# Kernel optimization log

Hardware: AMD Instinct MI355X
Metric: run time of the kernel (lower is better)

Reference implementation:

```python
import jax, jax.numpy as jnp
import numpy as np

S = 4096            # num tokens (single causal sequence)
HID = 1024          # hidden_size
NH = 16             # num query heads
NKV = 4             # num kv heads
HD = 64             # head_dim
THETA = 10000.0
Q_SIZE = NH * HD
KV_SIZE = NKV * HD


def setup_inputs() -> dict:
    key = jax.random.key(0)
    k1, k2, k3 = jax.random.split(key, 3)
    return {
        "positions": jnp.arange(S, dtype=jnp.int32),
        "hidden_states": jax.random.normal(k1, (S, 2 * HID), dtype=jnp.float32),
        "w_qkv": jax.random.normal(k2, (Q_SIZE + 2 * KV_SIZE, 2 * HID), dtype=jnp.float32) * 0.02,
        "w_o": jax.random.normal(k3, (HID, Q_SIZE), dtype=jnp.float32) * 0.02,
    }


def _rope(x, positions):
    # x: [S, H, HD]; neox-style rotate-half RoPE
    half = HD // 2
    inv_freq = 1.0 / (THETA ** (jnp.arange(0, half, dtype=jnp.float32) / half))
    freqs = positions.astype(jnp.float32)[:, None] * inv_freq  # [S, half]
    cos = jnp.cos(freqs)[:, None, :]  # [S, 1, half]
    sin = jnp.sin(freqs)[:, None, :]
    x1, x2 = x[..., :half], x[..., half:]
    return jnp.concatenate([x1 * cos - x2 * sin, x2 * cos + x1 * sin], axis=-1)


def reference(positions, hidden_states, w_qkv, w_o):
    qkv = hidden_states @ w_qkv.T  # [S, Q_SIZE + 2*KV_SIZE]
    q = qkv[:, :Q_SIZE].reshape(S, NH, HD)
    k = qkv[:, Q_SIZE:Q_SIZE + KV_SIZE].reshape(S, NKV, HD)
    v = qkv[:, Q_SIZE + KV_SIZE:].reshape(S, NKV, HD)
    q = _rope(q, positions)
    k = _rope(k, positions)
    # GQA: group query heads over kv heads
    g = NH // NKV
    qg = q.reshape(S, NKV, g, HD)
    scale = HD ** -0.5
    scores = jnp.einsum("qhgd,thd->hgqt", qg, k) * scale  # [NKV, g, S, S]
    causal = positions[:, None] >= positions[None, :]      # [S, S]
    scores = jnp.where(causal[None, None], scores, jnp.finfo(scores.dtype).min)
    probs = jax.nn.softmax(scores, axis=-1)
    o = jnp.einsum("hgqt,thd->qhgd", probs, v).reshape(S, Q_SIZE)
    return o @ w_o.T  # [S, HID]
```

## Files before the change

### kernel.cpp

```cpp
#include <hip/hip_runtime.h>
#include <math.h>

#define S_LEN   4096
#define NHEADS  16
#define NKVH    4
#define HDIM    64
#define QKV_N   1536
#define HID2    2048
#define OUT_N   1024

typedef __attribute__((ext_vector_type(8))) __bf16 bf16x8;
typedef __attribute__((ext_vector_type(4))) __bf16 bf16x4;
typedef __attribute__((ext_vector_type(4))) float  f32x4;
typedef __attribute__((ext_vector_type(16))) float f32x16;
typedef __attribute__((ext_vector_type(4))) unsigned int u32x4;

#define GL_LDS16(gaddr, laddr)                                                  \
  __builtin_amdgcn_global_load_lds(                                             \
      (const __attribute__((address_space(1))) unsigned int*)(gaddr),           \
      (__attribute__((address_space(3))) unsigned int*)(laddr), 16, 0, 0)

__device__ __forceinline__ unsigned cvt_pk_bf16(float lo, float hi) {
  unsigned r;
  asm("v_cvt_pk_bf16_f32 %0, %1, %2" : "=v"(r) : "v"(lo), "v"(hi));
  return r;
}

__global__ __launch_bounds__(256) void cvt_all(const float* __restrict__ hid,
                                               const float* __restrict__ wq,
                                               const float* __restrict__ wo,
                                               __bf16* __restrict__ hid_bf,
                                               __bf16* __restrict__ wq_bf,
                                               __bf16* __restrict__ wo_bf) {
  const int n1 = S_LEN * HID2;
  const int n2 = QKV_N * HID2;
  int i = (blockIdx.x * blockDim.x + threadIdx.x) * 8;
  const float* src; __bf16* dst; int off;
  if (i < n1)           { src = hid; dst = hid_bf; off = i; }
  else if (i < n1 + n2) { src = wq;  dst = wq_bf;  off = i - n1; }
  else                  { src = wo;  dst = wo_bf;  off = i - n1 - n2; }
  float4 a = *(const float4*)(src + off);
  float4 b = *(const float4*)(src + off + 4);
  bf16x8 o = {(__bf16)a.x,(__bf16)a.y,(__bf16)a.z,(__bf16)a.w,
              (__bf16)b.x,(__bf16)b.y,(__bf16)b.z,(__bf16)b.w};
  *(bf16x8*)(dst + off) = o;
}

__global__ __launch_bounds__(256) void rope_table(const int* __restrict__ positions,
                                                  float* __restrict__ ct,
                                                  float* __restrict__ st) {
  int i = blockIdx.x * blockDim.x + threadIdx.x;
  int s = i >> 5, d = i & 31;
  double inv = pow(10000.0, -(double)d / 32.0);
  double fr = (double)positions[s] * inv;
  ct[i] = (float)cos(fr);
  st[i] = (float)sin(fr);
}

template<int BM, bool C_BF16>
__global__ __launch_bounds__(256) void gemm_m97(const __bf16* __restrict__ A,
                                                const __bf16* __restrict__ B,
                                                void* __restrict__ Cp,
                                                int M, int N, int K) {
  constexpr int TM = BM / 32;
  __shared__ __align__(16) __bf16 As[BM * 32];
  __shared__ __align__(16) __bf16 Bs[128 * 32];
  const int tid  = threadIdx.x;
  const int bm   = blockIdx.x, bn = blockIdx.y;
  const int wave = tid >> 6, lane = tid & 63;
  const int quad = lane >> 4, col = lane & 15;
  const int wm = (wave >> 1) * (BM / 2), wn = (wave & 1) * 64;

  const int lrow = lane >> 2, lcol = (lane & 3) * 8;
  const __bf16* Ag = A + (size_t)(bm * BM + wave * (BM / 4) + lrow) * K + lcol;
  const __bf16* Bg = B + (size_t)(bn * 128 + wave * 32 + lrow) * K + lcol;
  __bf16* AsW = As + wave * (BM / 4) * 32;
  __bf16* BsW = Bs + wave * 32 * 32;

  f32x4 acc[TM][4];
#pragma unroll
  for (int i = 0; i < TM; ++i)
#pragma unroll
    for (int j = 0; j < 4; ++j) acc[i][j] = (f32x4){0.f, 0.f, 0.f, 0.f};

  for (int kk = 0; kk < K; kk += 32) {
    __syncthreads();
#pragma unroll
    for (int u = 0; u < BM / 64; ++u)
      GL_LDS16(Ag + kk + (size_t)(u * 16) * K, AsW + u * 16 * 32);
    GL_LDS16(Bg + kk,                  BsW);
    GL_LDS16(Bg + kk + (size_t)16 * K, BsW + 16 * 32);
    __syncthreads();

    bf16x8 a[TM], b[4];
#pragma unroll
    for (int tm = 0; tm < TM; ++tm)
      a[tm] = *(const bf16x8*)&As[(wm + tm * 16 + col) * 32 + quad * 8];
#pragma unroll
    for (int tn = 0; tn < 4; ++tn)
      b[tn] = *(const bf16x8*)&Bs[(wn + tn * 16 + col) * 32 + quad * 8];
#pragma unroll
    for (int tm = 0; tm < TM; ++tm)
#pragma unroll
      for (int tn = 0; tn < 4; ++tn)
        acc[tm][tn] = __builtin_amdgcn_mfma_f32_16x16x32_bf16(a[tm], b[tn], acc[tm][tn], 0, 0, 0);
  }

#pragma unroll
  for (int tm = 0; tm < TM; ++tm)
#pragma unroll
    for (int tn = 0; tn < 4; ++tn) {
      int row = bm * BM + wm + tm * 16 + quad * 4;
      int cg  = bn * 128 + wn + tn * 16 + col;
#pragma unroll
      for (int r = 0; r < 4; ++r) {
        if constexpr (C_BF16)
          ((__bf16*)Cp)[(size_t)(row + r) * N + cg] = (__bf16)acc[tm][tn][r];
        else
          ((float*)Cp)[(size_t)(row + r) * N + cg] = acc[tm][tn][r];
      }
    }
}

__global__ __launch_bounds__(256) void rope_cast(const __bf16* __restrict__ qkv,
                                                 const float* __restrict__ ct,
                                                 const float* __restrict__ st,
                                                 __bf16* __restrict__ qb,
                                                 __bf16* __restrict__ kb) {
  int g = blockIdx.x * blockDim.x + threadIdx.x;
  int d = g & 31;
  int rem = g >> 5;
  int head = rem % 20;
  int s = rem / 20;
  bool isq = head < NHEADS;
  const __bf16* src = qkv + (size_t)s * QKV_N + (isq ? head * 64 : 1024 + (head - 16) * 64);
  float c  = ct[s * 32 + d];
  float sn = st[s * 32 + d];
  float x1 = (float)src[d], x2 = (float)src[d + 32];
  float y1 = x1 * c - x2 * sn;
  float y2 = x2 * c + x1 * sn;
  float scl = isq ? 0.125f : 1.0f;
  __bf16* dst = isq ? (qb + (size_t)s * 1024 + head * 64)
                    : (kb + (size_t)s * 256 + (head - 16) * 64);
  dst[d]      = (__bf16)(y1 * scl);
  dst[d + 32] = (__bf16)(y2 * scl);
}

__global__ __launch_bounds__(256) void v_transpose(const __bf16* __restrict__ qkv,
                                                   __bf16* __restrict__ vT) {
  __shared__ __align__(16) __bf16 Ts[64][72];
  const int sb = blockIdx.x, kvh = blockIdx.y, t = threadIdx.x;
  const int r = t >> 2, c16 = (t & 3) * 16;
  const __bf16* src = qkv + (size_t)(sb * 64 + r) * QKV_N + 1280 + kvh * 64 + c16;
  bf16x8 v0 = *(const bf16x8*)src;
  bf16x8 v1 = *(const bf16x8*)(src + 8);
#pragma unroll
  for (int u = 0; u < 8; ++u) {
    Ts[c16 + u][r]     = v0[u];
    Ts[c16 + 8 + u][r] = v1[u];
  }
  __syncthreads();
  __bf16* dst = vT + ((size_t)kvh * 64 + r) * S_LEN + sb * 64 + c16;
  *(bf16x8*)dst       = *(const bf16x8*)&Ts[r][c16];
  *(bf16x8*)(dst + 8) = *(const bf16x8*)&Ts[r][c16 + 8];
}

__global__ __launch_bounds__(256, 4) void attn_split(const __bf16* __restrict__ qg,
                                                     const __bf16* __restrict__ kg,
                                                     const __bf16* __restrict__ vg,
                                                     __bf16* __restrict__ op0,
                                                     __bf16* __restrict__ op1,
                                                     float* __restrict__ lp) {
  __shared__ __align__(16) __bf16 lds[18432];
  __bf16* Ks = lds;
  __bf16* Vs = lds + 9216;

  const int tid = threadIdx.x;
  const int h = blockIdx.x;
  const int yy = blockIdx.y;
  const int qq = yy >> 1, split = yy & 1;
  const int qb = (qq < 16) ? qq : 47 - qq;
  const int kvh = h >> 2;
  const int wave = tid >> 6, lane = tid & 63;
  const int r31 = lane & 31, hi = lane >> 5;
  const int hi4 = hi * 4, hi8 = hi * 8;
  const int qbase = qb * 128 + wave * 32;
  const int kt0 = split * (qb + 1);
  const int ktEnd = kt0 + qb + 1;

  {
    const int r = tid >> 1, c = (tid & 1) * 32;
    const __bf16* src = qg + (size_t)(qb * 128 + r) * 1024 + h * 64 + c;
    __bf16* dq = lds + r * 72 + c;
    *(bf16x8*)(dq)      = *(const bf16x8*)(src);
    *(bf16x8*)(dq + 8)  = *(const bf16x8*)(src + 8);
    *(bf16x8*)(dq + 16) = *(const bf16x8*)(src + 16);
    *(bf16x8*)(dq + 24) = *(const bf16x8*)(src + 24);
  }

  const int sr = tid >> 2, sc = (tid & 3) * 16;
  const __bf16* kptr = kg + (size_t)sr * 256 + kvh * 64 + sc;
  const __bf16* vptr = vg + ((size_t)kvh * 64 + sr) * S_LEN + sc;
  bf16x8 kr0 = *(const bf16x8*)(kptr + (size_t)kt0 * 64 * 256);
  bf16x8 kr1 = *(const bf16x8*)(kptr + (size_t)kt0 * 64 * 256 + 8);
  bf16x8 vr0 = *(const bf16x8*)(vptr + (size_t)kt0 * 64);
  bf16x8 vr1 = *(const bf16x8*)(vptr + (size_t)kt0 * 64 + 8);

  __syncthreads();

  bf16x8 qf[4];
#pragma unroll
  for (int dc = 0; dc < 4; ++dc)
    qf[dc] = *(const bf16x8*)&lds[(wave * 32 + r31) * 72 + dc * 16 + hi8];

  __syncthreads();

  f32x16 o[2];
#pragma unroll
  for (int dt = 0; dt < 2; ++dt)
#pragma unroll
    for (int g = 0; g < 16; ++g) o[dt][g] = 0.f;
  float lacc = 0.f;

  for (int kt = kt0; kt < ktEnd; ++kt) {
    const int cur = (kt - kt0) & 1;
    {
      __bf16* kd = Ks + cur * 4608 + sr * 72 + sc;
      *(bf16x8*)kd       = kr0;
      *(bf16x8*)(kd + 8) = kr1;
      __bf16* vd = Vs + cur * 4608 + sr * 72 + sc;
      *(bf16x8*)vd       = vr0;
      *(bf16x8*)(vd + 8) = vr1;
    }
    if (kt + 1 < ktEnd) {
      const __bf16* kn = kptr + (size_t)(kt + 1) * 64 * 256;
      const __bf16* vn = vptr + (size_t)(kt + 1) * 64;
      kr0 = *(const bf16x8*)(kn);
      kr1 = *(const bf16x8*)(kn + 8);
      vr0 = *(const bf16x8*)(vn);
      vr1 = *(const bf16x8*)(vn + 8);
    }
    __syncthreads();

    if (kt * 64 > qbase + 31) continue;

    const bool full = (kt * 64 + 63 <= qbase);
    const int thr = qbase + r31 - kt * 64;

    bf16x8 pa[4];
#pragma unroll
    for (int kb = 0; kb < 2; ++kb) {
      f32x16 sf;
#pragma unroll
      for (int g = 0; g < 16; ++g) sf[g] = 0.f;
#pragma unroll
      for (int dc = 0; dc < 4; ++dc) {
        bf16x8 kf = *(const bf16x8*)&Ks[cur * 4608 + (kb * 32 + r31) * 72 + dc * 16 + hi8];
        sf = __builtin_amdgcn_mfma_f32_32x32x16_bf16(kf, qf[dc], sf, 0, 0, 0);
      }
      float p[16];
#pragma unroll
      for (int g = 0; g < 16; ++g) {
        float e = __expf(sf[g]);
        if (!full) {
          const int krow = kb * 32 + (g & 3) + 8 * (g >> 2) + hi4;
          if (krow > thr) e = 0.f;
        }
        p[g] = e;
      }
#pragma unroll
      for (int m = 0; m < 4; ++m)
        lacc += (p[4 * m] + p[4 * m + 1]) + (p[4 * m + 2] + p[4 * m + 3]);
#pragma unroll
      for (int half = 0; half < 2; ++half) {
        unsigned a0 = cvt_pk_bf16(p[8 * half + 0], p[8 * half + 1]);
        unsigned a1 = cvt_pk_bf16(p[8 * half + 2], p[8 * half + 3]);
        unsigned b0 = cvt_pk_bf16(p[8 * half + 4], p[8 * half + 5]);
        unsigned b1 = cvt_pk_bf16(p[8 * half + 6], p[8 * half + 7]);
        asm("v_permlane32_swap_b32 %0, %1" : "+v"(a0), "+v"(b0));
        asm("v_permlane32_swap_b32 %0, %1" : "+v"(a1), "+v"(b1));
        u32x4 t = {a0, a1, b0, b1};
        pa[kb * 2 + half] = __builtin_bit_cast(bf16x8, t);
      }
    }

#pragma unroll
    for (int dt = 0; dt < 2; ++dt)
#pragma unroll
      for (int kc = 0; kc < 4; ++kc) {
        bf16x8 vf = *(const bf16x8*)&Vs[cur * 4608 + (dt * 32 + r31) * 72 + kc * 16 + hi8];
        o[dt] = __builtin_amdgcn_mfma_f32_32x32x16_bf16(pa[kc], vf, o[dt], 0, 0, 0);
      }
  }

  lacc += __shfl_xor(lacc, 32, 64);
  __syncthreads();
  float* lshw = (float*)lds + wave * 32;
  if (lane < 32) lshw[lane] = lacc;
  asm volatile("s_waitcnt lgkmcnt(0)" ::: "memory");

  __bf16* op = split ? op1 : op0;
#pragma unroll
  for (int g = 0; g < 16; ++g) {
    const int rl = (g & 3) + 8 * (g >> 2) + hi4;
    float l = lshw[rl];
    float linv = (l > 0.f) ? 1.f / l : 0.f;
    const size_t row = (size_t)(qb * 128 + wave * 32 + rl);
    op[row * 1024 + h * 64 + r31]      = (__bf16)(o[0][g] * linv);
    op[row * 1024 + h * 64 + 32 + r31] = (__bf16)(o[1][g] * linv);
  }
  if (lane < 32)
    lp[(size_t)(split * S_LEN + qb * 128 + wave * 32 + lane) * NHEADS + h] = lacc;
}

__global__ __launch_bounds__(256) void attn_combine(const __bf16* __restrict__ op0,
                                                    const __bf16* __restrict__ op1,
                                                    const float* __restrict__ lp,
                                                    __bf16* __restrict__ ob) {
  int i = blockIdx.x * 256 + threadIdx.x;
  int row = i >> 7, c8 = (i & 127) * 8;
  int h = c8 >> 6;
  float l0 = lp[(size_t)row * NHEADS + h];
  float l1 = lp[(size_t)(S_LEN + row) * NHEADS + h];
  float inv = 1.f / (l0 + l1);
  float w0 = l0 * inv, w1 = l1 * inv;
  bf16x8 a = *(const bf16x8*)(op0 + (size_t)row * 1024 + c8);
  bf16x8 b = *(const bf16x8*)(op1 + (size_t)row * 1024 + c8);
  bf16x8 o;
#pragma unroll
  for (int u = 0; u < 8; ++u)
    o[u] = (__bf16)((float)a[u] * w0 + (float)b[u] * w1);
  *(bf16x8*)(ob + (size_t)row * 1024 + c8) = o;
}

extern "C" void kernel_launch(void* const* d_in, const int* in_sizes, int n_in,
                              void* d_out, int out_size, void* d_ws, size_t ws_size,
                              hipStream_t stream) {
  const int*   positions = (const int*)d_in[0];
  const float* hidden    = (const float*)d_in[1];
  const float* w_qkv     = (const float*)d_in[2];
  const float* w_o       = (const float*)d_in[3];
  float* out = (float*)d_out;

  char* ws = (char*)d_ws;
  __bf16* qkv_bf  = (__bf16*)ws;
  __bf16* Opart0  = (__bf16*)ws;
  __bf16* attn_bf = (__bf16*)ws;
  __bf16* hid_bf  = (__bf16*)(ws + 12582912);
  __bf16* q_bf    = (__bf16*)(ws + 12582912);
  __bf16* k_bf    = (__bf16*)(ws + 20971520);
  __bf16* vT      = (__bf16*)(ws + 23068672);
  float*  ct      = (float*)(ws + 29360128);
  float*  st      = (float*)(ws + 29884416);
  float*  lpart   = (float*)(ws + 29360128);
  __bf16* wq_bf   = (__bf16*)(ws + 30408704);
  __bf16* Opart1  = (__bf16*)(ws + 30408704);
  __bf16* wo_bf   = (__bf16*)(ws + 38797312);

  cvt_all<<<(S_LEN * HID2 + QKV_N * HID2 + OUT_N * OUT_N) / 8 / 256, 256, 0, stream>>>(
      hidden, w_qkv, w_o, hid_bf, wq_bf, wo_bf);
  rope_table<<<S_LEN * 32 / 256, 256, 0, stream>>>(positions, ct, st);

  gemm_m97<64, true><<<dim3(S_LEN / 64, QKV_N / 128), 256, 0, stream>>>(
      hid_bf, wq_bf, qkv_bf, S_LEN, QKV_N, HID2);

  rope_cast<<<(S_LEN * 20 * 32) / 256, 256, 0, stream>>>(qkv_bf, ct, st, q_bf, k_bf);
  v_transpose<<<dim3(S_LEN / 64, NKVH), 256, 0, stream>>>(qkv_bf, vT);

  attn_split<<<dim3(NHEADS, 64), 256, 0, stream>>>(q_bf, k_bf, vT, Opart0, Opart1, lpart);
  attn_combine<<<S_LEN * 128 / 256, 256, 0, stream>>>(Opart0, Opart1, lpart, attn_bf);

  gemm_m97<64, false><<<dim3(S_LEN / 64, OUT_N / 128), 256, 0, stream>>>(
      attn_bf, wo_bf, out, S_LEN, OUT_N, OUT_N);
}
```

Baseline: 228.3 us.

## Use exp2 with folded log2e scale, MFMA row sums, paired split jobs per block

Folds log2(e) into the Q scale so the softmax can use the native exp2 instruction instead of __expf. Row-sum accumulation moves from VALU adds plus a cross-lane shuffle and LDS exchange to an extra MFMA against a ones vector. Each block now runs two jobs (qb and 31-qb, first and second split halves) so causal work per block is balanced, and the grid is halved. Launch bounds drop to 2 waves per SIMD, giving more registers at the cost of occupancy. The bf16-rounded P sums may differ slightly from the fp32 sums used before.

```diff
diff --git a/kernel.cpp b/kernel.cpp
--- a/kernel.cpp
+++ b/kernel.cpp
@@ -139,7 +139,7 @@
   float x1 = (float)src[d], x2 = (float)src[d + 32];
   float y1 = x1 * c - x2 * sn;
   float y2 = x2 * c + x1 * sn;
-  float scl = isq ? 0.125f : 1.0f;
+  float scl = isq ? 0.18033688011112042f : 1.0f;
   __bf16* dst = isq ? (qb + (size_t)s * 1024 + head * 64)
                     : (kb + (size_t)s * 256 + (head - 16) * 64);
   dst[d]      = (__bf16)(y1 * scl);
@@ -165,7 +165,7 @@
   *(bf16x8*)(dst + 8) = *(const bf16x8*)&Ts[r][c16 + 8];
 }
 
-__global__ __launch_bounds__(256, 4) void attn_split(const __bf16* __restrict__ qg,
+__global__ __launch_bounds__(256, 2) void attn_split(const __bf16* __restrict__ qg,
                                                      const __bf16* __restrict__ kg,
                                                      const __bf16* __restrict__ vg,
                                                      __bf16* __restrict__ op0,
@@ -177,140 +177,146 @@
 
   const int tid = threadIdx.x;
   const int h = blockIdx.x;
-  const int yy = blockIdx.y;
-  const int qq = yy >> 1, split = yy & 1;
-  const int qb = (qq < 16) ? qq : 47 - qq;
+  const int qq = blockIdx.y;
   const int kvh = h >> 2;
   const int wave = tid >> 6, lane = tid & 63;
   const int r31 = lane & 31, hi = lane >> 5;
   const int hi4 = hi * 4, hi8 = hi * 8;
-  const int qbase = qb * 128 + wave * 32;
-  const int kt0 = split * (qb + 1);
-  const int ktEnd = kt0 + qb + 1;
-
-  {
-    const int r = tid >> 1, c = (tid & 1) * 32;
-    const __bf16* src = qg + (size_t)(qb * 128 + r) * 1024 + h * 64 + c;
-    __bf16* dq = lds + r * 72 + c;
-    *(bf16x8*)(dq)      = *(const bf16x8*)(src);
-    *(bf16x8*)(dq + 8)  = *(const bf16x8*)(src + 8);
-    *(bf16x8*)(dq + 16) = *(const bf16x8*)(src + 16);
-    *(bf16x8*)(dq + 24) = *(const bf16x8*)(src + 24);
-  }
-
   const int sr = tid >> 2, sc = (tid & 3) * 16;
   const __bf16* kptr = kg + (size_t)sr * 256 + kvh * 64 + sc;
   const __bf16* vptr = vg + ((size_t)kvh * 64 + sr) * S_LEN + sc;
-  bf16x8 kr0 = *(const bf16x8*)(kptr + (size_t)kt0 * 64 * 256);
-  bf16x8 kr1 = *(const bf16x8*)(kptr + (size_t)kt0 * 64 * 256 + 8);
-  bf16x8 vr0 = *(const bf16x8*)(vptr + (size_t)kt0 * 64);
-  bf16x8 vr1 = *(const bf16x8*)(vptr + (size_t)kt0 * 64 + 8);
-
-  __syncthreads();
-
-  bf16x8 qf[4];
-#pragma unroll
-  for (int dc = 0; dc < 4; ++dc)
-    qf[dc] = *(const bf16x8*)&lds[(wave * 32 + r31) * 72 + dc * 16 + hi8];
-
-  __syncthreads();
-
-  f32x16 o[2];
-#pragma unroll
-  for (int dt = 0; dt < 2; ++dt)
-#pragma unroll
-    for (int g = 0; g < 16; ++g) o[dt][g] = 0.f;
-  float lacc = 0.f;
-
-  for (int kt = kt0; kt < ktEnd; ++kt) {
-    const int cur = (kt - kt0) & 1;
+
+  f32x16 fz;
+#pragma unroll
+  for (int g = 0; g < 16; ++g) fz[g] = 0.f;
+  bf16x8 onesB;
+#pragma unroll
+  for (int u = 0; u < 8; ++u) onesB[u] = (__bf16)1.0f;
+
+  for (int job = 0; job < 2; ++job) {
+    const int qb = job ? (31 - qq) : qq;
+    const int qbase = qb * 128 + wave * 32;
+    const int kt0 = job * (qb + 1);
+    const int ktEnd = kt0 + qb + 1;
+
+    __syncthreads();
+
     {
-      __bf16* kd = Ks + cur * 4608 + sr * 72 + sc;
-      *(bf16x8*)kd       = kr0;
-      *(bf16x8*)(kd + 8) = kr1;
-      __bf16* vd = Vs + cur * 4608 + sr * 72 + sc;
-      *(bf16x8*)vd       = vr0;
-      *(bf16x8*)(vd + 8) = vr1;
-    }
-    if (kt + 1 < ktEnd) {
-      const __bf16* kn = kptr + (size_t)(kt + 1) * 64 * 256;
-      const __bf16* vn = vptr + (size_t)(kt + 1) * 64;
-      kr0 = *(const bf16x8*)(kn);
-      kr1 = *(const bf16x8*)(kn + 8);
-      vr0 = *(const bf16x8*)(vn);
-      vr1 = *(const bf16x8*)(vn + 8);
-    }
-    __syncthreads();
-
-    if (kt * 64 > qbase + 31) continue;
-
-    const bool full = (kt * 64 + 63 <= qbase);
-    const int thr = qbase + r31 - kt * 64;
-
-    bf16x8 pa[4];
-#pragma unroll
-    for (int kb = 0; kb < 2; ++kb) {
-      f32x16 sf;
-#pragma unroll
-      for (int g = 0; g < 16; ++g) sf[g] = 0.f;
-#pragma unroll
-      for (int dc = 0; dc < 4; ++dc) {
-        bf16x8 kf = *(const bf16x8*)&Ks[cur * 4608 + (kb * 32 + r31) * 72 + dc * 16 + hi8];
-        sf = __builtin_amdgcn_mfma_f32_32x32x16_bf16(kf, qf[dc], sf, 0, 0, 0);
-      }
-      float p[16];
+      const int r = tid >> 1, c = (tid & 1) * 32;
+      const __bf16* src = qg + (size_t)(qb * 128 + r) * 1024 + h * 64 + c;
+      __bf16* dq = lds + r * 72 + c;
+      *(bf16x8*)(dq)      = *(const bf16x8*)(src);
+      *(bf16x8*)(dq + 8)  = *(const bf16x8*)(src + 8);
+      *(bf16x8*)(dq + 16) = *(const bf16x8*)(src + 16);
+      *(bf16x8*)(dq + 24) = *(const bf16x8*)(src + 24);
+    }
+
+    bf16x8 kr0 = *(const bf16x8*)(kptr + (size_t)kt0 * 64 * 256);
+    bf16x8 kr1 = *(const bf16x8*)(kptr + (size_t)kt0 * 64 * 256 + 8);
+    bf16x8 vr0 = *(const bf16x8*)(vptr + (size_t)kt0 * 64);
+    bf16x8 vr1 = *(const bf16x8*)(vptr + (size_t)kt0 * 64 + 8);
+
+    __syncthreads();
+
+    bf16x8 qf[4];
+#pragma unroll
+    for (int dc = 0; dc < 4; ++dc)
+      qf[dc] = *(const bf16x8*)&lds[(wave * 32 + r31) * 72 + dc * 16 + hi8];
+
+    __syncthreads();
+
+    f32x16 o[2];
+    o[0] = fz; o[1] = fz;
+    f32x16 lones = fz;
+
+    for (int kt = kt0; kt < ktEnd; ++kt) {
+      const int cur = (kt - kt0) & 1;
+      {
+        __bf16* kd = Ks + cur * 4608 + sr * 72 + sc;
+        *(bf16x8*)kd       = kr0;
+        *(bf16x8*)(kd + 8) = kr1;
+        __bf16* vd = Vs + cur * 4608 + sr * 72 + sc;
+        *(bf16x8*)vd       = vr0;
+        *(bf16x8*)(vd + 8) = vr1;
+      }
+      if (kt + 1 < ktEnd) {
+        const __bf16* kn = kptr + (size_t)(kt + 1) * 64 * 256;
+        const __bf16* vn = vptr + (size_t)(kt + 1) * 64;
+        kr0 = *(const bf16x8*)(kn);
+        kr1 = *(const bf16x8*)(kn + 8);
+        vr0 = *(const bf16x8*)(vn);
+        vr1 = *(const bf16x8*)(vn + 8);
+      }
+      __syncthreads();
+
+      if (kt * 64 > qbase + 31) continue;
+
+      const bool full = (kt * 64 + 63 <= qbase);
+      const int thr = qbase + r31 - kt * 64;
+
+      bf16x8 pa[4];
+#pragma unroll
+      for (int kb = 0; kb < 2; ++kb) {
+        bf16x8 kf0 = *(const bf16x8*)&Ks[cur * 4608 + (kb * 32 + r31) * 72 + hi8];
+        f32x16 sf = __builtin_amdgcn_mfma_f32_32x32x16_bf16(kf0, qf[0], fz, 0, 0, 0);
+#pragma unroll
+        for (int dc = 1; dc < 4; ++dc) {
+          bf16x8 kf = *(const bf16x8*)&Ks[cur * 4608 + (kb * 32 + r31) * 72 + dc * 16 + hi8];
+          sf = __builtin_amdgcn_mfma_f32_32x32x16_bf16(kf, qf[dc], sf, 0, 0, 0);
+        }
+        float p[16];
+#pragma unroll
+        for (int g = 0; g < 16; ++g) {
+          float e = __builtin_amdgcn_exp2f(sf[g]);
+          if (!full) {
+            const int krow = kb * 32 + (g & 3) + 8 * (g >> 2) + hi4;
+            if (krow > thr) e = 0.f;
+          }
+          p[g] = e;
+        }
+#pragma unroll
+        for (int half = 0; half < 2; ++half) {
+          unsigned a0 = cvt_pk_bf16(p[8 * half + 0], p[8 * half + 1]);
+          unsigned a1 = cvt_pk_bf16(p[8 * half + 2], p[8 * half + 3]);
+          unsigned b0 = cvt_pk_bf16(p[8 * half + 4], p[8 * half + 5]);
+          unsigned b1 = cvt_pk_bf16(p[8 * half + 6], p[8 * half + 7]);
+          asm("v_permlane32_swap_b32 %0, %1" : "+v"(a0), "+v"(b0));
+          asm("v_permlane32_swap_b32 %0, %1" : "+v"(a1), "+v"(b1));
+          u32x4 t = {a0, a1, b0, b1};
+          pa[kb * 2 + half] = __builtin_bit_cast(bf16x8, t);
+        }
+      }
+
+#pragma unroll
+      for (int dt = 0; dt < 2; ++dt)
+#pragma unroll
+        for (int kc = 0; kc < 4; ++kc) {
+          bf16x8 vf = *(const bf16x8*)&Vs[cur * 4608 + (dt * 32 + r31) * 72 + kc * 16 + hi8];
+          o[dt] = __builtin_amdgcn_mfma_f32_32x32x16_bf16(pa[kc], vf, o[dt], 0, 0, 0);
+        }
+#pragma unroll
+      for (int kc = 0; kc < 4; ++kc)
+        lones = __builtin_amdgcn_mfma_f32_32x32x16_bf16(pa[kc], onesB, lones, 0, 0, 0);
+    }
+
+    __bf16* op = job ? op1 : op0;
+#pragma unroll
+    for (int g = 0; g < 16; ++g) {
+      const int rl = (g & 3) + 8 * (g >> 2) + hi4;
+      float l = lones[g];
+      float linv = (l > 0.f) ? 1.f / l : 0.f;
+      const size_t row = (size_t)(qb * 128 + wave * 32 + rl);
+      op[row * 1024 + h * 64 + r31]      = (__bf16)(o[0][g] * linv);
+      op[row * 1024 + h * 64 + 32 + r31] = (__bf16)(o[1][g] * linv);
+    }
+    if (r31 == 0) {
 #pragma unroll
       for (int g = 0; g < 16; ++g) {
-        float e = __expf(sf[g]);
-        if (!full) {
-          const int krow = kb * 32 + (g & 3) + 8 * (g >> 2) + hi4;
-          if (krow > thr) e = 0.f;
-        }
-        p[g] = e;
-      }
-#pragma unroll
-      for (int m = 0; m < 4; ++m)
-        lacc += (p[4 * m] + p[4 * m + 1]) + (p[4 * m + 2] + p[4 * m + 3]);
-#pragma unroll
-      for (int half = 0; half < 2; ++half) {
-        unsigned a0 = cvt_pk_bf16(p[8 * half + 0], p[8 * half + 1]);
-        unsigned a1 = cvt_pk_bf16(p[8 * half + 2], p[8 * half + 3]);
-        unsigned b0 = cvt_pk_bf16(p[8 * half + 4], p[8 * half + 5]);
-        unsigned b1 = cvt_pk_bf16(p[8 * half + 6], p[8 * half + 7]);
-        asm("v_permlane32_swap_b32 %0, %1" : "+v"(a0), "+v"(b0));
-        asm("v_permlane32_swap_b32 %0, %1" : "+v"(a1), "+v"(b1));
-        u32x4 t = {a0, a1, b0, b1};
-        pa[kb * 2 + half] = __builtin_bit_cast(bf16x8, t);
-      }
-    }
-
-#pragma unroll
-    for (int dt = 0; dt < 2; ++dt)
-#pragma unroll
-      for (int kc = 0; kc < 4; ++kc) {
-        bf16x8 vf = *(const bf16x8*)&Vs[cur * 4608 + (dt * 32 + r31) * 72 + kc * 16 + hi8];
-        o[dt] = __builtin_amdgcn_mfma_f32_32x32x16_bf16(pa[kc], vf, o[dt], 0, 0, 0);
-      }
+        const int rl = (g & 3) + 8 * (g >> 2) + hi4;
+        lp[(size_t)(job * S_LEN + qb * 128 + wave * 32 + rl) * NHEADS + h] = lones[g];
+      }
+    }
   }
-
-  lacc += __shfl_xor(lacc, 32, 64);
-  __syncthreads();
-  float* lshw = (float*)lds + wave * 32;
-  if (lane < 32) lshw[lane] = lacc;
-  asm volatile("s_waitcnt lgkmcnt(0)" ::: "memory");
-
-  __bf16* op = split ? op1 : op0;
-#pragma unroll
-  for (int g = 0; g < 16; ++g) {
-    const int rl = (g & 3) + 8 * (g >> 2) + hi4;
-    float l = lshw[rl];
-    float linv = (l > 0.f) ? 1.f / l : 0.f;
-    const size_t row = (size_t)(qb * 128 + wave * 32 + rl);
-    op[row * 1024 + h * 64 + r31]      = (__bf16)(o[0][g] * linv);
-    op[row * 1024 + h * 64 + 32 + r31] = (__bf16)(o[1][g] * linv);
-  }
-  if (lane < 32)
-    lp[(size_t)(split * S_LEN + qb * 128 + wave * 32 + lane) * NHEADS + h] = lacc;
 }
 
 __global__ __launch_bounds__(256) void attn_combine(const __bf16* __restrict__ op0,
@@ -367,7 +373,7 @@
   rope_cast<<<(S_LEN * 20 * 32) / 256, 256, 0, stream>>>(qkv_bf, ct, st, q_bf, k_bf);
   v_transpose<<<dim3(S_LEN / 64, NKVH), 256, 0, stream>>>(qkv_bf, vT);
 
-  attn_split<<<dim3(NHEADS, 64), 256, 0, stream>>>(q_bf, k_bf, vT, Opart0, Opart1, lpart);
+  attn_split<<<dim3(NHEADS, 32), 256, 0, stream>>>(q_bf, k_bf, vT, Opart0, Opart1, lpart);
   attn_combine<<<S_LEN * 128 / 256, 256, 0, stream>>>(Opart0, Opart1, lpart, attn_bf);
 
   gemm_m97<64, false><<<dim3(S_LEN / 64, OUT_N / 128), 256, 0, stream>>>(
```

After: 230.9 us. About the same (+1.1%).

## Split attention KV range three ways and fold log2e into Q scale

Applied to the files above, without the earlier changes.

Attention work now goes into three KV-range splits per query block instead of two paired splits, each an even share of the causal tiles. The combine kernel weights three partial outputs, and the third partial buffer lives in the output buffer. Softmax uses exp2 with log2(e) folded into the Q scale. The LDS double buffer becomes a single buffer with an extra barrier per tile, which cuts LDS use to raise occupancy but serialises load and compute. Some blocks may get an empty range, and there is more partial-result traffic.

```diff
diff --git a/kernel.cpp b/kernel.cpp
--- a/kernel.cpp
+++ b/kernel.cpp
@@ -139,7 +139,7 @@
   float x1 = (float)src[d], x2 = (float)src[d + 32];
   float y1 = x1 * c - x2 * sn;
   float y2 = x2 * c + x1 * sn;
-  float scl = isq ? 0.125f : 1.0f;
+  float scl = isq ? 0.18033688011112042f : 1.0f;
   __bf16* dst = isq ? (qb + (size_t)s * 1024 + head * 64)
                     : (kb + (size_t)s * 256 + (head - 16) * 64);
   dst[d]      = (__bf16)(y1 * scl);
@@ -170,23 +170,26 @@
                                                      const __bf16* __restrict__ vg,
                                                      __bf16* __restrict__ op0,
                                                      __bf16* __restrict__ op1,
+                                                     __bf16* __restrict__ op2,
                                                      float* __restrict__ lp) {
-  __shared__ __align__(16) __bf16 lds[18432];
+  __shared__ __align__(16) __bf16 lds[9216];
   __bf16* Ks = lds;
-  __bf16* Vs = lds + 9216;
+  __bf16* Vs = lds + 4608;
 
   const int tid = threadIdx.x;
   const int h = blockIdx.x;
-  const int yy = blockIdx.y;
-  const int qq = yy >> 1, split = yy & 1;
-  const int qb = (qq < 16) ? qq : 47 - qq;
+  const int qb = blockIdx.y;
+  const int cz = blockIdx.z;
   const int kvh = h >> 2;
   const int wave = tid >> 6, lane = tid & 63;
   const int r31 = lane & 31, hi = lane >> 5;
   const int hi4 = hi * 4, hi8 = hi * 8;
   const int qbase = qb * 128 + wave * 32;
-  const int kt0 = split * (qb + 1);
-  const int ktEnd = kt0 + qb + 1;
+
+  const int T = 2 * (qb + 1);
+  const int tb = T / 3, rm = T - 3 * tb;
+  const int kt0 = cz * tb + (cz < rm ? cz : rm);
+  const int ktEnd = kt0 + tb + (cz < rm ? 1 : 0);
 
   {
     const int r = tid >> 1, c = (tid & 1) * 32;
@@ -201,10 +204,13 @@
   const int sr = tid >> 2, sc = (tid & 3) * 16;
   const __bf16* kptr = kg + (size_t)sr * 256 + kvh * 64 + sc;
   const __bf16* vptr = vg + ((size_t)kvh * 64 + sr) * S_LEN + sc;
-  bf16x8 kr0 = *(const bf16x8*)(kptr + (size_t)kt0 * 64 * 256);
-  bf16x8 kr1 = *(const bf16x8*)(kptr + (size_t)kt0 * 64 * 256 + 8);
-  bf16x8 vr0 = *(const bf16x8*)(vptr + (size_t)kt0 * 64);
-  bf16x8 vr1 = *(const bf16x8*)(vptr + (size_t)kt0 * 64 + 8);
+  bf16x8 kr0, kr1, vr0, vr1;
+  if (kt0 < ktEnd) {
+    kr0 = *(const bf16x8*)(kptr + (size_t)kt0 * 64 * 256);
+    kr1 = *(const bf16x8*)(kptr + (size_t)kt0 * 64 * 256 + 8);
+    vr0 = *(const bf16x8*)(vptr + (size_t)kt0 * 64);
+    vr1 = *(const bf16x8*)(vptr + (size_t)kt0 * 64 + 8);
+  }
 
   __syncthreads();
 
@@ -223,12 +229,11 @@
   float lacc = 0.f;
 
   for (int kt = kt0; kt < ktEnd; ++kt) {
-    const int cur = (kt - kt0) & 1;
     {
-      __bf16* kd = Ks + cur * 4608 + sr * 72 + sc;
+      __bf16* kd = Ks + sr * 72 + sc;
       *(bf16x8*)kd       = kr0;
       *(bf16x8*)(kd + 8) = kr1;
-      __bf16* vd = Vs + cur * 4608 + sr * 72 + sc;
+      __bf16* vd = Vs + sr * 72 + sc;
       *(bf16x8*)vd       = vr0;
       *(bf16x8*)(vd + 8) = vr1;
     }
@@ -242,55 +247,56 @@
     }
     __syncthreads();
 
-    if (kt * 64 > qbase + 31) continue;
-
-    const bool full = (kt * 64 + 63 <= qbase);
-    const int thr = qbase + r31 - kt * 64;
-
-    bf16x8 pa[4];
-#pragma unroll
-    for (int kb = 0; kb < 2; ++kb) {
-      f32x16 sf;
-#pragma unroll
-      for (int g = 0; g < 16; ++g) sf[g] = 0.f;
-#pragma unroll
-      for (int dc = 0; dc < 4; ++dc) {
-        bf16x8 kf = *(const bf16x8*)&Ks[cur * 4608 + (kb * 32 + r31) * 72 + dc * 16 + hi8];
-        sf = __builtin_amdgcn_mfma_f32_32x32x16_bf16(kf, qf[dc], sf, 0, 0, 0);
+    if (kt * 64 <= qbase + 31) {
+      const bool full = (kt * 64 + 63 <= qbase);
+      const int thr = qbase + r31 - kt * 64;
+
+      bf16x8 pa[4];
+#pragma unroll
+      for (int kb = 0; kb < 2; ++kb) {
+        f32x16 sf;
+#pragma unroll
+        for (int g = 0; g < 16; ++g) sf[g] = 0.f;
+#pragma unroll
+        for (int dc = 0; dc < 4; ++dc) {
+          bf16x8 kf = *(const bf16x8*)&Ks[(kb * 32 + r31) * 72 + dc * 16 + hi8];
+          sf = __builtin_amdgcn_mfma_f32_32x32x16_bf16(kf, qf[dc], sf, 0, 0, 0);
+        }
+        float p[16];
+#pragma unroll
+        for (int g = 0; g < 16; ++g) {
+          float e = __builtin_amdgcn_exp2f(sf[g]);
+          if (!full) {
+            const int krow = kb * 32 + (g & 3) + 8 * (g >> 2) + hi4;
+            if (krow > thr) e = 0.f;
+          }
+          p[g] = e;
+        }
+#pragma unroll
+        for (int m = 0; m < 4; ++m)
+          lacc += (p[4 * m] + p[4 * m + 1]) + (p[4 * m + 2] + p[4 * m + 3]);
+#pragma unroll
+        for (int half = 0; half < 2; ++half) {
+          unsigned a0 = cvt_pk_bf16(p[8 * half + 0], p[8 * half + 1]);
+          unsigned a1 = cvt_pk_bf16(p[8 * half + 2], p[8 * half + 3]);
+          unsigned b0 = cvt_pk_bf16(p[8 * half + 4], p[8 * half + 5]);
+          unsigned b1 = cvt_pk_bf16(p[8 * half + 6], p[8 * half + 7]);
+          asm("v_permlane32_swap_b32 %0, %1" : "+v"(a0), "+v"(b0));
+          asm("v_permlane32_swap_b32 %0, %1" : "+v"(a1), "+v"(b1));
+          u32x4 t = {a0, a1, b0, b1};
+          pa[kb * 2 + half] = __builtin_bit_cast(bf16x8, t);
+        }
       }
-      float p[16];
-#pragma unroll
-      for (int g = 0; g < 16; ++g) {
-        float e = __expf(sf[g]);
-        if (!full) {
-          const int krow = kb * 32 + (g & 3) + 8 * (g >> 2) + hi4;
-          if (krow > thr) e = 0.f;
+
+#pragma unroll
+      for (int dt = 0; dt < 2; ++dt)
+#pragma unroll
+        for (int kc = 0; kc < 4; ++kc) {
+          bf16x8 vf = *(const bf16x8*)&Vs[(dt * 32 + r31) * 72 + kc * 16 + hi8];
+          o[dt] = __builtin_amdgcn_mfma_f32_32x32x16_bf16(pa[kc], vf, o[dt], 0, 0, 0);
         }
-        p[g] = e;
-      }
-#pragma unroll
-      for (int m = 0; m < 4; ++m)
-        lacc += (p[4 * m] + p[4 * m + 1]) + (p[4 * m + 2] + p[4 * m + 3]);
-#pragma unroll
-      for (int half = 0; half < 2; ++half) {
-        unsigned a0 = cvt_pk_bf16(p[8 * half + 0], p[8 * half + 1]);
-        unsigned a1 = cvt_pk_bf16(p[8 * half + 2], p[8 * half + 3]);
-        unsigned b0 = cvt_pk_bf16(p[8 * half + 4], p[8 * half + 5]);
-        unsigned b1 = cvt_pk_bf16(p[8 * half + 6], p[8 * half + 7]);
-        asm("v_permlane32_swap_b32 %0, %1" : "+v"(a0), "+v"(b0));
-        asm("v_permlane32_swap_b32 %0, %1" : "+v"(a1), "+v"(b1));
-        u32x4 t = {a0, a1, b0, b1};
-        pa[kb * 2 + half] = __builtin_bit_cast(bf16x8, t);
-      }
     }
-
-#pragma unroll
-    for (int dt = 0; dt < 2; ++dt)
-#pragma unroll
-      for (int kc = 0; kc < 4; ++kc) {
-        bf16x8 vf = *(const bf16x8*)&Vs[cur * 4608 + (dt * 32 + r31) * 72 + kc * 16 + hi8];
-        o[dt] = __builtin_amdgcn_mfma_f32_32x32x16_bf16(pa[kc], vf, o[dt], 0, 0, 0);
-      }
+    __syncthreads();
   }
 
   lacc += __shfl_xor(lacc, 32, 64);
@@ -299,7 +305,7 @@
   if (lane < 32) lshw[lane] = lacc;
   asm volatile("s_waitcnt lgkmcnt(0)" ::: "memory");
 
-  __bf16* op = split ? op1 : op0;
+  __bf16* op = (cz == 0) ? op0 : (cz == 1) ? op1 : op2;
 #pragma unroll
   for (int g = 0; g < 16; ++g) {
     const int rl = (g & 3) + 8 * (g >> 2) + hi4;
@@ -310,11 +316,12 @@
     op[row * 1024 + h * 64 + 32 + r31] = (__bf16)(o[1][g] * linv);
   }
   if (lane < 32)
-    lp[(size_t)(split * S_LEN + qb * 128 + wave * 32 + lane) * NHEADS + h] = lacc;
+    lp[(size_t)(cz * S_LEN + qb * 128 + wave * 32 + lane) * NHEADS + h] = lacc;
 }
 
 __global__ __launch_bounds__(256) void attn_combine(const __bf16* __restrict__ op0,
                                                     const __bf16* __restrict__ op1,
+                                                    const __bf16* __restrict__ op2,
                                                     const float* __restrict__ lp,
                                                     __bf16* __restrict__ ob) {
   int i = blockIdx.x * 256 + threadIdx.x;
@@ -322,14 +329,16 @@
   int h = c8 >> 6;
   float l0 = lp[(size_t)row * NHEADS + h];
   float l1 = lp[(size_t)(S_LEN + row) * NHEADS + h];
-  float inv = 1.f / (l0 + l1);
-  float w0 = l0 * inv, w1 = l1 * inv;
+  float l2 = lp[(size_t)(2 * S_LEN + row) * NHEADS + h];
+  float inv = 1.f / (l0 + l1 + l2);
+  float w0 = l0 * inv, w1 = l1 * inv, w2 = l2 * inv;
   bf16x8 a = *(const bf16x8*)(op0 + (size_t)row * 1024 + c8);
   bf16x8 b = *(const bf16x8*)(op1 + (size_t)row * 1024 + c8);
+  bf16x8 c = *(const bf16x8*)(op2 + (size_t)row * 1024 + c8);
   bf16x8 o;
 #pragma unroll
   for (int u = 0; u < 8; ++u)
-    o[u] = (__bf16)((float)a[u] * w0 + (float)b[u] * w1);
+    o[u] = (__bf16)((float)a[u] * w0 + (float)b[u] * w1 + (float)c[u] * w2);
   *(bf16x8*)(ob + (size_t)row * 1024 + c8) = o;
 }
 
@@ -346,16 +355,17 @@
   __bf16* qkv_bf  = (__bf16*)ws;
   __bf16* Opart0  = (__bf16*)ws;
   __bf16* attn_bf = (__bf16*)ws;
+  float*  lpart   = (float*)(ws + 8388608);
   __bf16* hid_bf  = (__bf16*)(ws + 12582912);
   __bf16* q_bf    = (__bf16*)(ws + 12582912);
   __bf16* k_bf    = (__bf16*)(ws + 20971520);
   __bf16* vT      = (__bf16*)(ws + 23068672);
   float*  ct      = (float*)(ws + 29360128);
   float*  st      = (float*)(ws + 29884416);
-  float*  lpart   = (float*)(ws + 29360128);
   __bf16* wq_bf   = (__bf16*)(ws + 30408704);
   __bf16* Opart1  = (__bf16*)(ws + 30408704);
   __bf16* wo_bf   = (__bf16*)(ws + 38797312);
+  __bf16* Opart2  = (__bf16*)d_out;
 
   cvt_all<<<(S_LEN * HID2 + QKV_N * HID2 + OUT_N * OUT_N) / 8 / 256, 256, 0, stream>>>(
       hidden, w_qkv, w_o, hid_bf, wq_bf, wo_bf);
@@ -367,8 +377,10 @@
   rope_cast<<<(S_LEN * 20 * 32) / 256, 256, 0, stream>>>(qkv_bf, ct, st, q_bf, k_bf);
   v_transpose<<<dim3(S_LEN / 64, NKVH), 256, 0, stream>>>(qkv_bf, vT);
 
-  attn_split<<<dim3(NHEADS, 64), 256, 0, stream>>>(q_bf, k_bf, vT, Opart0, Opart1, lpart);
-  attn_combine<<<S_LEN * 128 / 256, 256, 0, stream>>>(Opart0, Opart1, lpart, attn_bf);
+  attn_split<<<dim3(NHEADS, 32, 3), 256, 0, stream>>>(q_bf, k_bf, vT,
+                                                      Opart0, Opart1, Opart2, lpart);
+  attn_combine<<<S_LEN * 128 / 256, 256, 0, stream>>>(Opart0, Opart1, Opart2,
+                                                      lpart, attn_bf);
 
   gemm_m97<64, false><<<dim3(S_LEN / 64, OUT_N / 128), 256, 0, stream>>>(
       attn_bf, wo_bf, out, S_LEN, OUT_N, OUT_N);
```

New measurement: 241.5 us. 1.06x slower.

## Double-buffer GEMM LDS tiles and use exp2 with log2e-folded Q scale

Applied to the files above, without the earlier changes.

The GEMM now keeps two LDS buffers and issues the next K-slice's global-to-LDS loads before the MFMAs on the current slice, with one barrier per iteration instead of two. This is meant to overlap memory latency with compute. Attention folds log2(e) into the Q scaling so the softmax can use the hardware exp2 instead of __expf, and the first MFMA starts from a shared zero accumulator. The lpart buffer moves to a new workspace offset so it no longer aliases the rope tables. Double buffering doubles LDS per block, which may lower occupancy.

```diff
diff --git a/kernel.cpp b/kernel.cpp
--- a/kernel.cpp
+++ b/kernel.cpp
@@ -58,13 +58,13 @@
 }
 
 template<int BM, bool C_BF16>
-__global__ __launch_bounds__(256) void gemm_m97(const __bf16* __restrict__ A,
-                                                const __bf16* __restrict__ B,
-                                                void* __restrict__ Cp,
-                                                int M, int N, int K) {
+__global__ __launch_bounds__(256) void gemm_db(const __bf16* __restrict__ A,
+                                               const __bf16* __restrict__ B,
+                                               void* __restrict__ Cp,
+                                               int M, int N, int K) {
   constexpr int TM = BM / 32;
-  __shared__ __align__(16) __bf16 As[BM * 32];
-  __shared__ __align__(16) __bf16 Bs[128 * 32];
+  __shared__ __align__(16) __bf16 As[2 * BM * 32];
+  __shared__ __align__(16) __bf16 Bs[2 * 128 * 32];
   const int tid  = threadIdx.x;
   const int bm   = blockIdx.x, bn = blockIdx.y;
   const int wave = tid >> 6, lane = tid & 63;
@@ -83,27 +83,40 @@
 #pragma unroll
     for (int j = 0; j < 4; ++j) acc[i][j] = (f32x4){0.f, 0.f, 0.f, 0.f};
 
+#pragma unroll
+  for (int u = 0; u < BM / 64; ++u)
+    GL_LDS16(Ag + (size_t)(u * 16) * K, AsW + u * 16 * 32);
+  GL_LDS16(Bg,                  BsW);
+  GL_LDS16(Bg + (size_t)16 * K, BsW + 16 * 32);
+  __syncthreads();
+
+  int cur = 0;
   for (int kk = 0; kk < K; kk += 32) {
-    __syncthreads();
-#pragma unroll
-    for (int u = 0; u < BM / 64; ++u)
-      GL_LDS16(Ag + kk + (size_t)(u * 16) * K, AsW + u * 16 * 32);
-    GL_LDS16(Bg + kk,                  BsW);
-    GL_LDS16(Bg + kk + (size_t)16 * K, BsW + 16 * 32);
-    __syncthreads();
+    if (kk + 32 < K) {
+      const int nxt = cur ^ 1;
+#pragma unroll
+      for (int u = 0; u < BM / 64; ++u)
+        GL_LDS16(Ag + kk + 32 + (size_t)(u * 16) * K,
+                 AsW + nxt * BM * 32 + u * 16 * 32);
+      GL_LDS16(Bg + kk + 32,                  BsW + nxt * 128 * 32);
+      GL_LDS16(Bg + kk + 32 + (size_t)16 * K, BsW + nxt * 128 * 32 + 16 * 32);
+    }
 
     bf16x8 a[TM], b[4];
 #pragma unroll
     for (int tm = 0; tm < TM; ++tm)
-      a[tm] = *(const bf16x8*)&As[(wm + tm * 16 + col) * 32 + quad * 8];
+      a[tm] = *(const bf16x8*)&As[cur * BM * 32 + (wm + tm * 16 + col) * 32 + quad * 8];
 #pragma unroll
     for (int tn = 0; tn < 4; ++tn)
-      b[tn] = *(const bf16x8*)&Bs[(wn + tn * 16 + col) * 32 + quad * 8];
+      b[tn] = *(const bf16x8*)&Bs[cur * 128 * 32 + (wn + tn * 16 + col) * 32 + quad * 8];
 #pragma unroll
     for (int tm = 0; tm < TM; ++tm)
 #pragma unroll
       for (int tn = 0; tn < 4; ++tn)
         acc[tm][tn] = __builtin_amdgcn_mfma_f32_16x16x32_bf16(a[tm], b[tn], acc[tm][tn], 0, 0, 0);
+
+    __syncthreads();
+    cur ^= 1;
   }
 
 #pragma unroll
@@ -139,7 +152,7 @@
   float x1 = (float)src[d], x2 = (float)src[d + 32];
   float y1 = x1 * c - x2 * sn;
   float y2 = x2 * c + x1 * sn;
-  float scl = isq ? 0.125f : 1.0f;
+  float scl = isq ? 0.18033688011112042f : 1.0f;
   __bf16* dst = isq ? (qb + (size_t)s * 1024 + head * 64)
                     : (kb + (size_t)s * 256 + (head - 16) * 64);
   dst[d]      = (__bf16)(y1 * scl);
@@ -215,11 +228,12 @@
 
   __syncthreads();
 
+  f32x16 fz;
+#pragma unroll
+  for (int g = 0; g < 16; ++g) fz[g] = 0.f;
+
   f32x16 o[2];
-#pragma unroll
-  for (int dt = 0; dt < 2; ++dt)
-#pragma unroll
-    for (int g = 0; g < 16; ++g) o[dt][g] = 0.f;
+  o[0] = fz; o[1] = fz;
   float lacc = 0.f;
 
   for (int kt = kt0; kt < ktEnd; ++kt) {
@@ -250,18 +264,17 @@
     bf16x8 pa[4];
 #pragma unroll
     for (int kb = 0; kb < 2; ++kb) {
-      f32x16 sf;
-#pragma unroll
-      for (int g = 0; g < 16; ++g) sf[g] = 0.f;
-#pragma unroll
-      for (int dc = 0; dc < 4; ++dc) {
+      bf16x8 kf0 = *(const bf16x8*)&Ks[cur * 4608 + (kb * 32 + r31) * 72 + hi8];
+      f32x16 sf = __builtin_amdgcn_mfma_f32_32x32x16_bf16(kf0, qf[0], fz, 0, 0, 0);
+#pragma unroll
+      for (int dc = 1; dc < 4; ++dc) {
         bf16x8 kf = *(const bf16x8*)&Ks[cur * 4608 + (kb * 32 + r31) * 72 + dc * 16 + hi8];
         sf = __builtin_amdgcn_mfma_f32_32x32x16_bf16(kf, qf[dc], sf, 0, 0, 0);
       }
       float p[16];
 #pragma unroll
       for (int g = 0; g < 16; ++g) {
-        float e = __expf(sf[g]);
+        float e = __builtin_amdgcn_exp2f(sf[g]);
         if (!full) {
           const int krow = kb * 32 + (g & 3) + 8 * (g >> 2) + hi4;
           if (krow > thr) e = 0.f;
@@ -346,13 +359,13 @@
   __bf16* qkv_bf  = (__bf16*)ws;
   __bf16* Opart0  = (__bf16*)ws;
   __bf16* attn_bf = (__bf16*)ws;
+  float*  lpart   = (float*)(ws + 8388608);
   __bf16* hid_bf  = (__bf16*)(ws + 12582912);
   __bf16* q_bf    = (__bf16*)(ws + 12582912);
   __bf16* k_bf    = (__bf16*)(ws + 20971520);
   __bf16* vT      = (__bf16*)(ws + 23068672);
   float*  ct      = (float*)(ws + 29360128);
   float*  st      = (float*)(ws + 29884416);
-  float*  lpart   = (float*)(ws + 29360128);
   __bf16* wq_bf   = (__bf16*)(ws + 30408704);
   __bf16* Opart1  = (__bf16*)(ws + 30408704);
   __bf16* wo_bf   = (__bf16*)(ws + 38797312);
@@ -361,15 +374,16 @@
       hidden, w_qkv, w_o, hid_bf, wq_bf, wo_bf);
   rope_table<<<S_LEN * 32 / 256, 256, 0, stream>>>(positions, ct, st);
 
-  gemm_m97<64, true><<<dim3(S_LEN / 64, QKV_N / 128), 256, 0, stream>>>(
+  gemm_db<64, true><<<dim3(S_LEN / 64, QKV_N / 128), 256, 0, stream>>>(
       hid_bf, wq_bf, qkv_bf, S_LEN, QKV_N, HID2);
 
   rope_cast<<<(S_LEN * 20 * 32) / 256, 256, 0, stream>>>(qkv_bf, ct, st, q_bf, k_bf);
   v_transpose<<<dim3(S_LEN / 64, NKVH), 256, 0, stream>>>(qkv_bf, vT);
 
-  attn_split<<<dim3(NHEADS, 64), 256, 0, stream>>>(q_bf, k_bf, vT, Opart0, Opart1, lpart);
+  attn_split<<<dim3(NHEADS, 64), 256, 0, stream>>>(q_bf, k_bf, vT,
+                                                   Opart0, Opart1, lpart);
   attn_combine<<<S_LEN * 128 / 256, 256, 0, stream>>>(Opart0, Opart1, lpart, attn_bf);
 
-  gemm_m97<64, false><<<dim3(S_LEN / 64, OUT_N / 128), 256, 0, stream>>>(
+  gemm_db<64, false><<<dim3(S_LEN / 64, OUT_N / 128), 256, 0, stream>>>(
       attn_bf, wo_bf, out, S_LEN, OUT_N, OUT_N);
 }
```

Measured after the change: 221.9 us. -2.8%, faster.
